# Performance work log

Hardware: AMD Instinct MI355X
Metric: run time of the kernel (lower is better)

The kernel has to match this reference:

```python
import jax, jax.numpy as jnp
import numpy as np

EPS = 1e-12  # F.normalize eps


def setup_inputs() -> dict:
    key = jax.random.key(0)
    k1, k2 = jax.random.split(key)
    bs, d = 8192, 128
    data = jax.random.normal(k1, (bs, d), dtype=jnp.float32)
    label = jax.random.randint(k2, (bs, 1), 0, 2, dtype=jnp.int64)
    scale = jnp.asarray(np.log(1.0 / 0.07), dtype=jnp.float32)  # learned temperature param
    return {"data": data, "scale": scale, "label": label}


def reference(data, scale, label):
    bs = data.shape[0]
    # L2-normalize rows (F.normalize semantics with eps clamp)
    norm = jnp.maximum(jnp.linalg.norm(data, axis=-1, keepdims=True), EPS)
    x = data / norm
    logits = (x @ x.T) * jnp.exp(scale)  # [bs, bs]
    # Vectorized equivalent of the python double loop: binary same-class matrix
    sim = (label == label.T).astype(logits.dtype)  # [bs, bs]
    q = jax.nn.softmax(sim / jnp.sum(sim, axis=-1, keepdims=True), axis=-1)
    p = jax.nn.log_softmax(logits, axis=-1)
    log_q = jnp.log(q)  # q > 0 always (softmax output)
    # F.kl_div(p, q, 'batchmean') = sum(q * (log q - p)) / bs
    loss1 = jnp.sum(q * (log_q - p)) / bs
    # F.kl_div(q.log(), p.exp(), 'batchmean') = sum(exp(p) * (p - log q)) / bs
    loss2 = jnp.sum(jnp.exp(p) * (p - log_q)) / bs
    return (loss1 + loss2) * 0.5
```

## Files before the change

### kernel.cpp

```cpp
#include <hip/hip_runtime.h>
#include <stdint.h>

#define BS 8192
#define DD 128
#define L2E 1.4426950408889634f
#define LN2 0.6931471805599453f

typedef __attribute__((ext_vector_type(8))) short short8;
typedef __attribute__((ext_vector_type(4))) float float4v;

#if __has_builtin(__builtin_amdgcn_exp2f)
#define EXP2(x) __builtin_amdgcn_exp2f(x)
#else
#define EXP2(x) exp2f(x)
#endif

__device__ __forceinline__ float bf2f(short s) {
  union { unsigned u; float f; } c;
  c.u = ((unsigned)(unsigned short)s) << 16;
  return c.f;
}
__device__ __forceinline__ short f2bf(float f) {
  union { float f; unsigned u; } c; c.f = f;
  unsigned u = c.u + 0x7FFFu + ((c.u >> 16) & 1u);
  return (short)(u >> 16);
}


__global__ __launch_bounds__(256) void k_norm(const float* __restrict__ data,
                                              const int* __restrict__ label,
                                              char* __restrict__ xnbF,
                                              float* __restrict__ gh4,
                                              int* __restrict__ cnt4,
                                              float* __restrict__ Zr,
                                              float* __restrict__ Ur,
                                              float* __restrict__ Vr,
                                              float* __restrict__ mf) {
  __shared__ float shg[256];
  __shared__ int shc[2];
  int tid = threadIdx.x, wave = tid >> 6, lane = tid & 63;
  int lh = lane & 31, rsel = lane >> 5;
  if (tid < 2) shc[tid] = 0;
  shg[tid] = 0.f;
  int rowbase = blockIdx.x * 32;
  if (tid < 32) {
    int row = rowbase + tid;
    Zr[row] = 0.f; Ur[row] = 0.f; Vr[row] = 0.f;
    mf[row] = (label[row] == 0) ? 1.f : 0.f;
  }
  __syncthreads();

  float a00 = 0.f, a01 = 0.f, a02 = 0.f, a03 = 0.f;
  float a10 = 0.f, a11 = 0.f, a12 = 0.f, a13 = 0.f;
  int c0 = 0, c1 = 0;
#pragma unroll
  for (int it = 0; it < 4; ++it) {
    int row = rowbase + it * 8 + wave * 2 + rsel;
    float4 v = *(const float4*)&data[row * DD + lh * 4];
    float ss = v.x * v.x + v.y * v.y + v.z * v.z + v.w * v.w;
#pragma unroll
    for (int off = 16; off; off >>= 1) ss += __shfl_xor(ss, off);
    float rn = 1.f / fmaxf(sqrtf(ss), 1e-12f);
    float x0 = v.x * rn, x1 = v.y * rn, x2 = v.z * rn, x3 = v.w * rn;

    unsigned pk0 = (unsigned)(unsigned short)f2bf(x0) |
                   ((unsigned)(unsigned short)f2bf(x1) << 16);
    unsigned pk1 = (unsigned)(unsigned short)f2bf(x2) |
                   ((unsigned)(unsigned short)f2bf(x3) << 16);
    int kc = lh >> 1;
    size_t chunk = (size_t)(row >> 4) * 256 + (size_t)(kc >> 2) * 64 +
                   (size_t)(kc & 3) * 16 + (row & 15);
    *(uint2*)(xnbF + chunk * 16 + (lh & 1) * 8) = make_uint2(pk0, pk1);

    int lab = label[row];
    if (lab == 0) {
      a00 += x0; a01 += x1; a02 += x2; a03 += x3;
      if (lh == 0) c0++;
    } else {
      a10 += x0; a11 += x1; a12 += x2; a13 += x3;
      if (lh == 0) c1++;
    }
  }
  int base = lh * 4;
  atomicAdd(&shg[base + 0], a00); atomicAdd(&shg[base + 1], a01);
  atomicAdd(&shg[base + 2], a02); atomicAdd(&shg[base + 3], a03);
  atomicAdd(&shg[128 + base + 0], a10); atomicAdd(&shg[128 + base + 1], a11);
  atomicAdd(&shg[128 + base + 2], a12); atomicAdd(&shg[128 + base + 3], a13);
  if (lh == 0) { atomicAdd(&shc[0], c0); atomicAdd(&shc[1], c1); }
  __syncthreads();
  atomicAdd(&gh4[(blockIdx.x & 3) * 256 + tid], shg[tid]);
  if (tid < 2) atomicAdd(&cnt4[(blockIdx.x & 3) * 2 + tid], shc[tid]);
}

__global__ __launch_bounds__(256, 2) void k_main(const short* __restrict__ xnbF,
                                                 const int* __restrict__ label,
                                                 const float* __restrict__ mf,
                                                 const float* __restrict__ scale,
                                                 float* __restrict__ Zr,
                                                 float* __restrict__ Ur,
                                                 float* __restrict__ Vr) {
  int tid = threadIdx.x, wave = tid >> 6, lane = tid & 63;
  int quad = lane >> 4, col = lane & 15;
  int rbI = blockIdx.x >> 5;
  int sl = blockIdx.x & 31;
  float se2 = __expf(scale[0]) * L2E;

  const short8* F = (const short8*)xnbF;

  int gA = rbI * 16 + wave * 4;
  short8 af[4][4];
#pragma unroll
  for (int s = 0; s < 4; ++s)
#pragma unroll
    for (int t = 0; t < 4; ++t) {
      short8 a = F[(size_t)(gA + s) * 256 + t * 64 + lane];
#pragma unroll
      for (int i = 0; i < 8; ++i) a[i] = f2bf(bf2f(a[i]) * se2);
      asm volatile("" : "+v"(a));
      af[s][t] = a;
    }

  float4v Zc0 = {0.f,0.f,0.f,0.f}, Zc1 = Zc0, Zc2 = Zc0, Zc3 = Zc0;
  float4v Uc0 = Zc0, Uc1 = Zc0, Uc2 = Zc0, Uc3 = Zc0;
  float4v Vc0 = Zc0, Vc1 = Zc0, Vc2 = Zc0, Vc3 = Zc0;

  const short8* FB = F + (size_t)(sl * 16) * 256 + lane;
  short8 n0 = FB[0], n1 = FB[64], n2 = FB[128], n3 = FB[192];
  float nm = mf[sl * 256 + col];

#pragma unroll 1
  for (int gg = 0; gg < 16; ++gg) {
    short8 b0 = n0, b1 = n1, b2 = n2, b3 = n3;
    float bm = nm;
    if (gg < 15) {
      const short8* np = FB + (size_t)(gg + 1) * 256;
      n0 = np[0]; n1 = np[64]; n2 = np[128]; n3 = np[192];
      nm = mf[sl * 256 + (gg + 1) * 16 + col];
    }
#define ROWSET(s, Zc, Uc, Vc)                                                  \
    {                                                                          \
      float4v c = {0.f, 0.f, 0.f, 0.f};                                        \
      c = __builtin_amdgcn_mfma_f32_16x16x32_bf16(af[s][0], b0, c, 0, 0, 0);   \
      c = __builtin_amdgcn_mfma_f32_16x16x32_bf16(af[s][1], b1, c, 0, 0, 0);   \
      c = __builtin_amdgcn_mfma_f32_16x16x32_bf16(af[s][2], b2, c, 0, 0, 0);   \
      c = __builtin_amdgcn_mfma_f32_16x16x32_bf16(af[s][3], b3, c, 0, 0, 0);   \
      _Pragma("unroll")                                                        \
      for (int r = 0; r < 4; ++r) {  \
        float l = c[r], e = EXP2(l);    \
        Zc[r] += e;                                                            \
        Uc[r] = fmaf(e, l, Uc[r]);                                             \
        Vc[r] = fmaf(bm, e, Vc[r]);                                            \
      }                                                                        \
    }
    ROWSET(0, Zc0, Uc0, Vc0)
    ROWSET(1, Zc1, Uc1, Vc1)
    ROWSET(2, Zc2, Uc2, Vc2)
    ROWSET(3, Zc3, Uc3, Vc3)
#undef ROWSET
  }

#define EMIT(s, Zc, Uc, Vc)                                                    \
  {                                                                            \
    _Pragma("unroll")                                                          \
    for (int r = 0; r < 4; ++r) {                                              \
      float z = Zc[r], u = Uc[r], v0 = Vc[r];                                  \
      _Pragma("unroll")                                                        \
      for (int off = 1; off < 16; off <<= 1) {                                 \
        z += __shfl_xor(z, off);                                               \
        u += __shfl_xor(u, off);                                               \
        v0 += __shfl_xor(v0, off);                                             \
      }                                                                        \
      if (col == 0) {                                                          \
        int row = rbI * 256 + wave * 64 + s * 16 + quad * 4 + r;               \
        int lab = label[row];                                                  \
        float v = (lab == 0) ? v0 : (z - v0);                                  \
        atomicAdd(&Zr[row], z);                                                \
        atomicAdd(&Ur[row], u * LN2);                 \
        atomicAdd(&Vr[row], v);                                                \
      }                                                                        \
    }                                                                          \
  }
  EMIT(0, Zc0, Uc0, Vc0)
  EMIT(1, Zc1, Uc1, Vc1)
  EMIT(2, Zc2, Uc2, Vc2)
  EMIT(3, Zc3, Uc3, Vc3)
#undef EMIT
}

__global__ __launch_bounds__(256) void k_final(const float* __restrict__ data,
                                               const int* __restrict__ label,
                                               const float* __restrict__ scale,
                                               const float* __restrict__ gh4,
                                               const int* __restrict__ cnt4,
                                               const float* __restrict__ Zr,
                                               const float* __restrict__ Ur,
                                               const float* __restrict__ Vr,
                                               float* __restrict__ partial) {
  __shared__ float hsum[256];
  __shared__ float bsum[4];
  int tid = threadIdx.x, wave = tid >> 6, lane = tid & 63;
  int lh = lane & 31, rsel = lane >> 5;
  hsum[tid] = gh4[tid] + gh4[256 + tid] + gh4[512 + tid] + gh4[768 + tid];
  __syncthreads();

  float se = __expf(scale[0]);
  float c0 = (float)(cnt4[0] + cnt4[2] + cnt4[4] + cnt4[6]);
  float c1 = (float)(cnt4[1] + cnt4[3] + cnt4[5] + cnt4[7]);
  float4 h0 = *(const float4*)&hsum[lh * 4];
  float4 h1 = *(const float4*)&hsum[128 + lh * 4];

  float local = 0.f;
#pragma unroll
  for (int it = 0; it < 4; ++it) {
    int row = blockIdx.x * 32 + it * 8 + wave * 2 + rsel;
    float4 v = *(const float4*)&data[row * DD + lh * 4];
    float ss = v.x * v.x + v.y * v.y + v.z * v.z + v.w * v.w;
#pragma unroll
    for (int off = 16; off; off >>= 1) ss += __shfl_xor(ss, off);
    float rn = 1.f / fmaxf(sqrtf(ss), 1e-12f);

    int lab = label[row];
    float sg = v.x * (h0.x + h1.x) + v.y * (h0.y + h1.y) +
               v.z * (h0.z + h1.z) + v.w * (h0.w + h1.w);
    float sh_ = (lab == 0)
                    ? (v.x * h0.x + v.y * h0.y + v.z * h0.z + v.w * h0.w)
                    : (v.x * h1.x + v.y * h1.y + v.z * h1.z + v.w * h1.w);
#pragma unroll
    for (int off = 16; off; off >>= 1) {
      sg += __shfl_xor(sg, off);
      sh_ += __shfl_xor(sh_, off);
    }
    if (lh == 0) {
      float cc = (lab == 0) ? c0 : c1;
      float a = __expf(1.f / cc);
      float Zq = cc * a + ((float)BS - cc);
      float S = se * sg * rn, T = se * sh_ * rn;
      float Zv = Zr[row], Uv = Ur[row], Vv = Vr[row];
      local += a / Zq - (S + (a - 1.f) * T) / Zq + Uv / Zv - Vv / (cc * Zv);
    }
  }
#pragma unroll
  for (int off = 32; off; off >>= 1) local += __shfl_xor(local, off);
  if (lane == 0) bsum[wave] = local;
  __syncthreads();
  if (tid == 0) partial[blockIdx.x] = bsum[0] + bsum[1] + bsum[2] + bsum[3];
}

__global__ __launch_bounds__(256) void k_sum(const float* __restrict__ partial,
                                             float* __restrict__ out) {
  __shared__ float bsum[4];
  int tid = threadIdx.x, wave = tid >> 6, lane = tid & 63;
  float v = partial[tid];
#pragma unroll
  for (int off = 32; off; off >>= 1) v += __shfl_xor(v, off);
  if (lane == 0) bsum[wave] = v;
  __syncthreads();
  if (tid == 0)
    out[0] = (bsum[0] + bsum[1] + bsum[2] + bsum[3]) * (0.5f / (float)BS);
}

extern "C" void kernel_launch(void* const* d_in, const int* in_sizes, int n_in,
                              void* d_out, int out_size, void* d_ws, size_t ws_size,
                              hipStream_t stream) {
  const float* data = (const float*)d_in[0];
  const float* scale = (const float*)d_in[1];
  const int* label = (const int*)d_in[2];
  char* ws = (char*)d_ws;
  char* xnbF = ws;
  float* Zr = (float*)(ws + 2097152);
  float* Ur = (float*)(ws + 2129920);
  float* Vr = (float*)(ws + 2162688);
  float* gh4 = (float*)(ws + 2195456);
  int* cnt4 = (int*)(ws + 2199552);
  float* mf = (float*)(ws + 2199584);
  float* partial = (float*)(ws + 2232352);

  hipMemsetAsync(ws + 2195456, 0, 4128, stream);

  k_norm<<<256, 256, 0, stream>>>(data, label, xnbF, gh4, cnt4, Zr, Ur, Vr, mf);
  k_main<<<1024, 256, 0, stream>>>((const short*)xnbF, label, mf, scale, Zr, Ur, Vr);
  k_final<<<256, 256, 0, stream>>>(data, label, scale, gh4, cnt4, Zr, Ur, Vr, partial);
  k_sum<<<1, 256, 0, stream>>>(partial, (float*)d_out);
}
```

Measured before the change: 122.4 us.

## Software-pipeline MFMA with exp epilogue and fuse final sum into last block

The main loop is restructured into a two-stage ping-pong: the MFMAs for one column group are issued while the exp/accumulate epilogue of the previous group runs, and B tiles are prefetched two groups ahead. The goal is to overlap matrix-core latency with the transcendental epilogue. Separately, the k_sum launch is removed by having the last k_final block, chosen with an atomic ticket, do the final reduction. The asm barrier on the A fragments is also dropped. These changes add register pressure and an acquire/release handshake in exchange.

Result: no change. 124.8 us (+1.9%).

```diff
diff --git a/kernel.cpp b/kernel.cpp
--- a/kernel.cpp
+++ b/kernel.cpp
@@ -116,7 +116,6 @@
       short8 a = F[(size_t)(gA + s) * 256 + t * 64 + lane];
 #pragma unroll
       for (int i = 0; i < 8; ++i) a[i] = f2bf(bf2f(a[i]) * se2);
-      asm volatile("" : "+v"(a));
       af[s][t] = a;
     }
 
@@ -125,39 +124,64 @@
   float4v Vc0 = Zc0, Vc1 = Zc0, Vc2 = Zc0, Vc3 = Zc0;
 
   const short8* FB = F + (size_t)(sl * 16) * 256 + lane;
-  short8 n0 = FB[0], n1 = FB[64], n2 = FB[128], n3 = FB[192];
-  float nm = mf[sl * 256 + col];
-
+  const float* MB = mf + sl * 256 + col;
+
+  short8 pA0, pA1, pA2, pA3, pB0, pB1, pB2, pB3;
+  float mA, mB_;
+  float4v cP0, cP1, cP2, cP3, cQ0, cQ1, cQ2, cQ3;
+
+#define LOADP(g) { const short8* p_ = FB + (size_t)(g) * 256;                  \
+    pA0 = p_[0]; pA1 = p_[64]; pA2 = p_[128]; pA3 = p_[192];                   \
+    mA = MB[(g) * 16]; }
+#define LOADQ(g) { const short8* p_ = FB + (size_t)(g) * 256;                  \
+    pB0 = p_[0]; pB1 = p_[64]; pB2 = p_[128]; pB3 = p_[192];                   \
+    mB_ = MB[(g) * 16]; }
+#define MFMA1(cc, s, b0, b1, b2, b3)                                           \
+    cc = (float4v){0.f, 0.f, 0.f, 0.f};                                        \
+    cc = __builtin_amdgcn_mfma_f32_16x16x32_bf16(af[s][0], b0, cc, 0, 0, 0);   \
+    cc = __builtin_amdgcn_mfma_f32_16x16x32_bf16(af[s][1], b1, cc, 0, 0, 0);   \
+    cc = __builtin_amdgcn_mfma_f32_16x16x32_bf16(af[s][2], b2, cc, 0, 0, 0);   \
+    cc = __builtin_amdgcn_mfma_f32_16x16x32_bf16(af[s][3], b3, cc, 0, 0, 0);
+#define MFMA4(c0, c1, c2, c3, b0, b1, b2, b3)                                  \
+    { MFMA1(c0, 0, b0, b1, b2, b3) MFMA1(c1, 1, b0, b1, b2, b3)                \
+      MFMA1(c2, 2, b0, b1, b2, b3) MFMA1(c3, 3, b0, b1, b2, b3) }
+#define EPIROW(cc, Zc, Uc, Vc, mm)                                             \
+    { _Pragma("unroll")                                                        \
+      for (int r = 0; r < 4; ++r) {  \
+        float l = (cc)[r], e = EXP2(l);      \
+        (Zc)[r] += e;                                                          \
+        (Uc)[r] = fmaf(e, l, (Uc)[r]);                                         \
+        (Vc)[r] = fmaf((mm), e, (Vc)[r]);                                      \
+      } }
+#define EPI4(c0, c1, c2, c3, mm)                                               \
+    EPIROW(c0, Zc0, Uc0, Vc0, mm) EPIROW(c1, Zc1, Uc1, Vc1, mm)                \
+    EPIROW(c2, Zc2, Uc2, Vc2, mm) EPIROW(c3, Zc3, Uc3, Vc3, mm)
+
+  LOADP(0); LOADQ(1);
+  MFMA4(cP0, cP1, cP2, cP3, pA0, pA1, pA2, pA3);
+  float mPe = mA;
+  LOADP(2);
 #pragma unroll 1
-  for (int gg = 0; gg < 16; ++gg) {
-    short8 b0 = n0, b1 = n1, b2 = n2, b3 = n3;
-    float bm = nm;
-    if (gg < 15) {
-      const short8* np = FB + (size_t)(gg + 1) * 256;
-      n0 = np[0]; n1 = np[64]; n2 = np[128]; n3 = np[192];
-      nm = mf[sl * 256 + (gg + 1) * 16 + col];
-    }
-#define ROWSET(s, Zc, Uc, Vc)                                                  \
-    {                                                                          \
-      float4v c = {0.f, 0.f, 0.f, 0.f};                                        \
-      c = __builtin_amdgcn_mfma_f32_16x16x32_bf16(af[s][0], b0, c, 0, 0, 0);   \
-      c = __builtin_amdgcn_mfma_f32_16x16x32_bf16(af[s][1], b1, c, 0, 0, 0);   \
-      c = __builtin_amdgcn_mfma_f32_16x16x32_bf16(af[s][2], b2, c, 0, 0, 0);   \
-      c = __builtin_amdgcn_mfma_f32_16x16x32_bf16(af[s][3], b3, c, 0, 0, 0);   \
-      _Pragma("unroll")                                                        \
-      for (int r = 0; r < 4; ++r) {  \
-        float l = c[r], e = EXP2(l);    \
-        Zc[r] += e;                                                            \
-        Uc[r] = fmaf(e, l, Uc[r]);                                             \
-        Vc[r] = fmaf(bm, e, Vc[r]);                                            \
-      }                                                                        \
-    }
-    ROWSET(0, Zc0, Uc0, Vc0)
-    ROWSET(1, Zc1, Uc1, Vc1)
-    ROWSET(2, Zc2, Uc2, Vc2)
-    ROWSET(3, Zc3, Uc3, Vc3)
-#undef ROWSET
-  }
+  for (int g = 1; g < 14; g += 2) {
+    MFMA4(cQ0, cQ1, cQ2, cQ3, pB0, pB1, pB2, pB3);
+    float mQe = mB_;
+    LOADQ(g + 2);
+    EPI4(cP0, cP1, cP2, cP3, mPe);
+    MFMA4(cP0, cP1, cP2, cP3, pA0, pA1, pA2, pA3);
+    mPe = mA;
+    if (g + 3 < 16) LOADP(g + 3);
+    EPI4(cQ0, cQ1, cQ2, cQ3, mQe);
+  }
+  MFMA4(cQ0, cQ1, cQ2, cQ3, pB0, pB1, pB2, pB3);
+  float mQe = mB_;
+  EPI4(cP0, cP1, cP2, cP3, mPe);
+  EPI4(cQ0, cQ1, cQ2, cQ3, mQe);
+#undef LOADP
+#undef LOADQ
+#undef MFMA1
+#undef MFMA4
+#undef EPIROW
+#undef EPI4
 
 #define EMIT(s, Zc, Uc, Vc)                                                    \
   {                                                                            \
@@ -195,9 +219,12 @@
                                                const float* __restrict__ Zr,
                                                const float* __restrict__ Ur,
                                                const float* __restrict__ Vr,
-                                               float* __restrict__ partial) {
+                                               float* __restrict__ partial,
+                                               int* __restrict__ ticket,
+                                               float* __restrict__ out) {
   __shared__ float hsum[256];
   __shared__ float bsum[4];
+  __shared__ int lastb;
   int tid = threadIdx.x, wave = tid >> 6, lane = tid & 63;
   int lh = lane & 31, rsel = lane >> 5;
   hsum[tid] = gh4[tid] + gh4[256 + tid] + gh4[512 + tid] + gh4[768 + tid];
@@ -243,20 +270,25 @@
   for (int off = 32; off; off >>= 1) local += __shfl_xor(local, off);
   if (lane == 0) bsum[wave] = local;
   __syncthreads();
-  if (tid == 0) partial[blockIdx.x] = bsum[0] + bsum[1] + bsum[2] + bsum[3];
-}
-
-__global__ __launch_bounds__(256) void k_sum(const float* __restrict__ partial,
-                                             float* __restrict__ out) {
-  __shared__ float bsum[4];
-  int tid = threadIdx.x, wave = tid >> 6, lane = tid & 63;
-  float v = partial[tid];
-#pragma unroll
-  for (int off = 32; off; off >>= 1) v += __shfl_xor(v, off);
-  if (lane == 0) bsum[wave] = v;
-  __syncthreads();
-  if (tid == 0)
-    out[0] = (bsum[0] + bsum[1] + bsum[2] + bsum[3]) * (0.5f / (float)BS);
+  if (tid == 0) {
+    float psum = bsum[0] + bsum[1] + bsum[2] + bsum[3];
+    __hip_atomic_store(&partial[blockIdx.x], psum, __ATOMIC_RELEASE,
+                       __HIP_MEMORY_SCOPE_AGENT);
+    int t = __hip_atomic_fetch_add(ticket, 1, __ATOMIC_ACQ_REL,
+                                   __HIP_MEMORY_SCOPE_AGENT);
+    lastb = (t == 255);
+  }
+  __syncthreads();
+  if (lastb) {
+    float v = __hip_atomic_load(&partial[tid], __ATOMIC_ACQUIRE,
+                                __HIP_MEMORY_SCOPE_AGENT);
+#pragma unroll
+    for (int off = 32; off; off >>= 1) v += __shfl_xor(v, off);
+    if (lane == 0) bsum[wave] = v;
+    __syncthreads();
+    if (tid == 0)
+      out[0] = (bsum[0] + bsum[1] + bsum[2] + bsum[3]) * (0.5f / (float)BS);
+  }
 }
 
 extern "C" void kernel_launch(void* const* d_in, const int* in_sizes, int n_in,
@@ -272,13 +304,14 @@
   float* Vr = (float*)(ws + 2162688);
   float* gh4 = (float*)(ws + 2195456);
   int* cnt4 = (int*)(ws + 2199552);
-  float* mf = (float*)(ws + 2199584);
-  float* partial = (float*)(ws + 2232352);
-
-  hipMemsetAsync(ws + 2195456, 0, 4128, stream);
+  int* ticket = (int*)(ws + 2199584);
+  float* partial = (float*)(ws + 2199588);
+  float* mf = (float*)(ws + 2200640);
+
+  hipMemsetAsync(ws + 2195456, 0, 4132, stream);
 
   k_norm<<<256, 256, 0, stream>>>(data, label, xnbF, gh4, cnt4, Zr, Ur, Vr, mf);
   k_main<<<1024, 256, 0, stream>>>((const short*)xnbF, label, mf, scale, Zr, Ur, Vr);
-  k_final<<<256, 256, 0, stream>>>(data, label, scale, gh4, cnt4, Zr, Ur, Vr, partial);
-  k_sum<<<1, 256, 0, stream>>>(partial, (float*)d_out);
-}
+  k_final<<<256, 256, 0, stream>>>(data, label, scale, gh4, cnt4, Zr, Ur, Vr,
+                                   partial, ticket, (float*)d_out);
+}
```

## Stage B tiles in LDS via global_load_lds, widen blocks, fuse final sum

Applied to the files above, without the earlier changes.

The main GEMM-softmax kernel now runs 512-thread blocks whose 8 waves share double-buffered LDS tiles of the column operand, loaded with direct global-to-LDS instructions. Each wave holds 2 row groups instead of 4 and computes a 2x2 MFMA grid per step, so each column fragment is reused across row groups and global traffic for B drops. The separate reduction kernel is folded into k_final through an atomic ticket that lets the last block finish the sum, saving one launch. Histogram partials are spread over 8 slots instead of 4 to cut atomic contention, at the cost of more LDS use, extra block-wide syncs, and fewer independent rows per wave.

Result: faster. 108.7 us (-11.2%).

```diff
diff --git a/kernel.cpp b/kernel.cpp
--- a/kernel.cpp
+++ b/kernel.cpp
@@ -30,8 +30,8 @@
 __global__ __launch_bounds__(256) void k_norm(const float* __restrict__ data,
                                               const int* __restrict__ label,
                                               char* __restrict__ xnbF,
-                                              float* __restrict__ gh4,
-                                              int* __restrict__ cnt4,
+                                              float* __restrict__ gh8,
+                                              int* __restrict__ cnt8,
                                               float* __restrict__ Zr,
                                               float* __restrict__ Ur,
                                               float* __restrict__ Vr,
@@ -88,76 +88,113 @@
   atomicAdd(&shg[128 + base + 2], a12); atomicAdd(&shg[128 + base + 3], a13);
   if (lh == 0) { atomicAdd(&shc[0], c0); atomicAdd(&shc[1], c1); }
   __syncthreads();
-  atomicAdd(&gh4[(blockIdx.x & 3) * 256 + tid], shg[tid]);
-  if (tid < 2) atomicAdd(&cnt4[(blockIdx.x & 3) * 2 + tid], shc[tid]);
-}
-
-__global__ __launch_bounds__(256, 2) void k_main(const short* __restrict__ xnbF,
+  atomicAdd(&gh8[(blockIdx.x & 7) * 256 + tid], shg[tid]);
+  if (tid < 2) atomicAdd(&cnt8[(blockIdx.x & 7) * 2 + tid], shc[tid]);
+}
+
+__global__ __launch_bounds__(512, 4) void k_main(const short* __restrict__ xnbF,
                                                  const int* __restrict__ label,
                                                  const float* __restrict__ mf,
                                                  const float* __restrict__ scale,
                                                  float* __restrict__ Zr,
                                                  float* __restrict__ Ur,
                                                  float* __restrict__ Vr) {
+  __shared__ short tile[2][64 * DD];
   int tid = threadIdx.x, wave = tid >> 6, lane = tid & 63;
   int quad = lane >> 4, col = lane & 15;
-  int rbI = blockIdx.x >> 5;
-  int sl = blockIdx.x & 31;
+  int rbI = blockIdx.x >> 4;
+  int sl = blockIdx.x & 15;
   float se2 = __expf(scale[0]) * L2E;
 
   const short8* F = (const short8*)xnbF;
 
-  int gA = rbI * 16 + wave * 4;
-  short8 af[4][4];
-#pragma unroll
-  for (int s = 0; s < 4; ++s)
+  int gA = rbI * 16 + wave * 2;
+  short8 af[2][4];
+#pragma unroll
+  for (int s = 0; s < 2; ++s)
 #pragma unroll
     for (int t = 0; t < 4; ++t) {
       short8 a = F[(size_t)(gA + s) * 256 + t * 64 + lane];
 #pragma unroll
       for (int i = 0; i < 8; ++i) a[i] = f2bf(bf2f(a[i]) * se2);
-      asm volatile("" : "+v"(a));
       af[s][t] = a;
     }
 
-  float4v Zc0 = {0.f,0.f,0.f,0.f}, Zc1 = Zc0, Zc2 = Zc0, Zc3 = Zc0;
-  float4v Uc0 = Zc0, Uc1 = Zc0, Uc2 = Zc0, Uc3 = Zc0;
-  float4v Vc0 = Zc0, Vc1 = Zc0, Vc2 = Zc0, Vc3 = Zc0;
-
-  const short8* FB = F + (size_t)(sl * 16) * 256 + lane;
-  short8 n0 = FB[0], n1 = FB[64], n2 = FB[128], n3 = FB[192];
-  float nm = mf[sl * 256 + col];
+  float4v Z0 = {0.f,0.f,0.f,0.f}, Z1 = Z0, U0 = Z0, U1 = Z0, V0 = Z0, V1 = Z0;
+
+  int cb4 = sl * 32;
+
+#define STAGE(buf, jt)                                                         \
+  {                                                                            \
+    const char* s_ = (const char*)xnbF +                                       \
+                     ((size_t)(cb4 + (jt) * 4) * 256 + tid) * 16;              \
+    char* d_ = (char*)tile[buf] + tid * 16;                                    \
+    __builtin_amdgcn_global_load_lds(                                          \
+        (const __attribute__((address_space(1))) void*)(uintptr_t)s_,          \
+        (__attribute__((address_space(3))) void*)(uintptr_t)d_, 16, 0, 0);     \
+    __builtin_amdgcn_global_load_lds(                                          \
+        (const __attribute__((address_space(1))) void*)(uintptr_t)(s_ + 8192), \
+        (__attribute__((address_space(3))) void*)(uintptr_t)(d_ + 8192),       \
+        16, 0, 0);                                                             \
+  }
+
+  STAGE(0, 0);
+  __syncthreads();
 
 #pragma unroll 1
-  for (int gg = 0; gg < 16; ++gg) {
-    short8 b0 = n0, b1 = n1, b2 = n2, b3 = n3;
-    float bm = nm;
-    if (gg < 15) {
-      const short8* np = FB + (size_t)(gg + 1) * 256;
-      n0 = np[0]; n1 = np[64]; n2 = np[128]; n3 = np[192];
-      nm = mf[sl * 256 + (gg + 1) * 16 + col];
-    }
-#define ROWSET(s, Zc, Uc, Vc)                                                  \
+  for (int jt = 0; jt < 8; ++jt) {
+    if (jt < 7) STAGE((jt + 1) & 1, jt + 1);
+    const short8* T8 = (const short8*)tile[jt & 1];
+    int jcb = sl * 512 + jt * 64;
+
+#define HALFTILE(jo)                                                           \
     {                                                                          \
-      float4v c = {0.f, 0.f, 0.f, 0.f};                                        \
-      c = __builtin_amdgcn_mfma_f32_16x16x32_bf16(af[s][0], b0, c, 0, 0, 0);   \
-      c = __builtin_amdgcn_mfma_f32_16x16x32_bf16(af[s][1], b1, c, 0, 0, 0);   \
-      c = __builtin_amdgcn_mfma_f32_16x16x32_bf16(af[s][2], b2, c, 0, 0, 0);   \
-      c = __builtin_amdgcn_mfma_f32_16x16x32_bf16(af[s][3], b3, c, 0, 0, 0);   \
+      short8 b00 = T8[(jo) * 256 + lane];                                      \
+      short8 b01 = T8[(jo) * 256 + 64 + lane];                                 \
+      short8 b02 = T8[(jo) * 256 + 128 + lane];                                \
+      short8 b03 = T8[(jo) * 256 + 192 + lane];                                \
+      short8 b10 = T8[(jo + 1) * 256 + lane];                                  \
+      short8 b11 = T8[(jo + 1) * 256 + 64 + lane];                             \
+      short8 b12 = T8[(jo + 1) * 256 + 128 + lane];                            \
+      short8 b13 = T8[(jo + 1) * 256 + 192 + lane];                            \
+      float m0 = mf[jcb + (jo) * 16 + col];                                    \
+      float m1 = mf[jcb + (jo + 1) * 16 + col];                                \
+      float4v c00 = {0.f, 0.f, 0.f, 0.f}, c01 = c00, c10 = c00, c11 = c00;     \
+      c00 = __builtin_amdgcn_mfma_f32_16x16x32_bf16(af[0][0], b00, c00, 0,0,0);\
+      c01 = __builtin_amdgcn_mfma_f32_16x16x32_bf16(af[1][0], b00, c01, 0,0,0);\
+      c10 = __builtin_amdgcn_mfma_f32_16x16x32_bf16(af[0][0], b10, c10, 0,0,0);\
+      c11 = __builtin_amdgcn_mfma_f32_16x16x32_bf16(af[1][0], b10, c11, 0,0,0);\
+      c00 = __builtin_amdgcn_mfma_f32_16x16x32_bf16(af[0][1], b01, c00, 0,0,0);\
+      c01 = __builtin_amdgcn_mfma_f32_16x16x32_bf16(af[1][1], b01, c01, 0,0,0);\
+      c10 = __builtin_amdgcn_mfma_f32_16x16x32_bf16(af[0][1], b11, c10, 0,0,0);\
+      c11 = __builtin_amdgcn_mfma_f32_16x16x32_bf16(af[1][1], b11, c11, 0,0,0);\
+      c00 = __builtin_amdgcn_mfma_f32_16x16x32_bf16(af[0][2], b02, c00, 0,0,0);\
+      c01 = __builtin_amdgcn_mfma_f32_16x16x32_bf16(af[1][2], b02, c01, 0,0,0);\
+      c10 = __builtin_amdgcn_mfma_f32_16x16x32_bf16(af[0][2], b12, c10, 0,0,0);\
+      c11 = __builtin_amdgcn_mfma_f32_16x16x32_bf16(af[1][2], b12, c11, 0,0,0);\
+      c00 = __builtin_amdgcn_mfma_f32_16x16x32_bf16(af[0][3], b03, c00, 0,0,0);\
+      c01 = __builtin_amdgcn_mfma_f32_16x16x32_bf16(af[1][3], b03, c01, 0,0,0);\
+      c10 = __builtin_amdgcn_mfma_f32_16x16x32_bf16(af[0][3], b13, c10, 0,0,0);\
+      c11 = __builtin_amdgcn_mfma_f32_16x16x32_bf16(af[1][3], b13, c11, 0,0,0);\
       _Pragma("unroll")                                                        \
       for (int r = 0; r < 4; ++r) {  \
-        float l = c[r], e = EXP2(l);    \
-        Zc[r] += e;                                                            \
-        Uc[r] = fmaf(e, l, Uc[r]);                                             \
-        Vc[r] = fmaf(bm, e, Vc[r]);                                            \
+        float l, e;                                                            \
+        l = c00[r]; e = EXP2(l);        \
+        Z0[r] += e; U0[r] = fmaf(e, l, U0[r]); V0[r] = fmaf(m0, e, V0[r]);     \
+        l = c01[r]; e = EXP2(l);                                               \
+        Z1[r] += e; U1[r] = fmaf(e, l, U1[r]); V1[r] = fmaf(m0, e, V1[r]);     \
+        l = c10[r]; e = EXP2(l);                                               \
+        Z0[r] += e; U0[r] = fmaf(e, l, U0[r]); V0[r] = fmaf(m1, e, V0[r]);     \
+        l = c11[r]; e = EXP2(l);                                               \
+        Z1[r] += e; U1[r] = fmaf(e, l, U1[r]); V1[r] = fmaf(m1, e, V1[r]);     \
       }                                                                        \
     }
-    ROWSET(0, Zc0, Uc0, Vc0)
-    ROWSET(1, Zc1, Uc1, Vc1)
-    ROWSET(2, Zc2, Uc2, Vc2)
-    ROWSET(3, Zc3, Uc3, Vc3)
-#undef ROWSET
-  }
+    HALFTILE(0)
+    HALFTILE(2)
+#undef HALFTILE
+    __syncthreads();
+  }
+#undef STAGE
 
 #define EMIT(s, Zc, Uc, Vc)                                                    \
   {                                                                            \
@@ -171,7 +208,7 @@
         v0 += __shfl_xor(v0, off);                                             \
       }                                                                        \
       if (col == 0) {                                                          \
-        int row = rbI * 256 + wave * 64 + s * 16 + quad * 4 + r;               \
+        int row = rbI * 256 + wave * 32 + s * 16 + quad * 4 + r;               \
         int lab = label[row];                                                  \
         float v = (lab == 0) ? v0 : (z - v0);                                  \
         atomicAdd(&Zr[row], z);                                                \
@@ -180,32 +217,38 @@
       }                                                                        \
     }                                                                          \
   }
-  EMIT(0, Zc0, Uc0, Vc0)
-  EMIT(1, Zc1, Uc1, Vc1)
-  EMIT(2, Zc2, Uc2, Vc2)
-  EMIT(3, Zc3, Uc3, Vc3)
+  EMIT(0, Z0, U0, V0)
+  EMIT(1, Z1, U1, V1)
 #undef EMIT
 }
 
 __global__ __launch_bounds__(256) void k_final(const float* __restrict__ data,
                                                const int* __restrict__ label,
                                                const float* __restrict__ scale,
-                                               const float* __restrict__ gh4,
-                                               const int* __restrict__ cnt4,
+                                               const float* __restrict__ gh8,
+                                               const int* __restrict__ cnt8,
                                                const float* __restrict__ Zr,
                                                const float* __restrict__ Ur,
                                                const float* __restrict__ Vr,
-                                               float* __restrict__ partial) {
+                                               float* __restrict__ partial,
+                                               int* __restrict__ ticket,
+                                               float* __restrict__ out) {
   __shared__ float hsum[256];
   __shared__ float bsum[4];
+  __shared__ int lastb;
   int tid = threadIdx.x, wave = tid >> 6, lane = tid & 63;
   int lh = lane & 31, rsel = lane >> 5;
-  hsum[tid] = gh4[tid] + gh4[256 + tid] + gh4[512 + tid] + gh4[768 + tid];
+  float hs = 0.f;
+#pragma unroll
+  for (int i = 0; i < 8; ++i) hs += gh8[i * 256 + tid];
+  hsum[tid] = hs;
   __syncthreads();
 
   float se = __expf(scale[0]);
-  float c0 = (float)(cnt4[0] + cnt4[2] + cnt4[4] + cnt4[6]);
-  float c1 = (float)(cnt4[1] + cnt4[3] + cnt4[5] + cnt4[7]);
+  int ci0 = 0, ci1 = 0;
+#pragma unroll
+  for (int i = 0; i < 8; ++i) { ci0 += cnt8[2 * i]; ci1 += cnt8[2 * i + 1]; }
+  float c0 = (float)ci0, c1 = (float)ci1;
   float4 h0 = *(const float4*)&hsum[lh * 4];
   float4 h1 = *(const float4*)&hsum[128 + lh * 4];
 
@@ -243,20 +286,25 @@
   for (int off = 32; off; off >>= 1) local += __shfl_xor(local, off);
   if (lane == 0) bsum[wave] = local;
   __syncthreads();
-  if (tid == 0) partial[blockIdx.x] = bsum[0] + bsum[1] + bsum[2] + bsum[3];
-}
-
-__global__ __launch_bounds__(256) void k_sum(const float* __restrict__ partial,
-                                             float* __restrict__ out) {
-  __shared__ float bsum[4];
-  int tid = threadIdx.x, wave = tid >> 6, lane = tid & 63;
-  float v = partial[tid];
-#pragma unroll
-  for (int off = 32; off; off >>= 1) v += __shfl_xor(v, off);
-  if (lane == 0) bsum[wave] = v;
-  __syncthreads();
-  if (tid == 0)
-    out[0] = (bsum[0] + bsum[1] + bsum[2] + bsum[3]) * (0.5f / (float)BS);
+  if (tid == 0) {
+    float psum = bsum[0] + bsum[1] + bsum[2] + bsum[3];
+    __hip_atomic_store(&partial[blockIdx.x], psum, __ATOMIC_RELEASE,
+                       __HIP_MEMORY_SCOPE_AGENT);
+    int t = __hip_atomic_fetch_add(ticket, 1, __ATOMIC_ACQ_REL,
+                                   __HIP_MEMORY_SCOPE_AGENT);
+    lastb = (t == 255);
+  }
+  __syncthreads();
+  if (lastb) {
+    float v = __hip_atomic_load(&partial[tid], __ATOMIC_ACQUIRE,
+                                __HIP_MEMORY_SCOPE_AGENT);
+#pragma unroll
+    for (int off = 32; off; off >>= 1) v += __shfl_xor(v, off);
+    if (lane == 0) bsum[wave] = v;
+    __syncthreads();
+    if (tid == 0)
+      out[0] = (bsum[0] + bsum[1] + bsum[2] + bsum[3]) * (0.5f / (float)BS);
+  }
 }
 
 extern "C" void kernel_launch(void* const* d_in, const int* in_sizes, int n_in,
@@ -270,15 +318,16 @@
   float* Zr = (float*)(ws + 2097152);
   float* Ur = (float*)(ws + 2129920);
   float* Vr = (float*)(ws + 2162688);
-  float* gh4 = (float*)(ws + 2195456);
-  int* cnt4 = (int*)(ws + 2199552);
-  float* mf = (float*)(ws + 2199584);
-  float* partial = (float*)(ws + 2232352);
-
-  hipMemsetAsync(ws + 2195456, 0, 4128, stream);
-
-  k_norm<<<256, 256, 0, stream>>>(data, label, xnbF, gh4, cnt4, Zr, Ur, Vr, mf);
-  k_main<<<1024, 256, 0, stream>>>((const short*)xnbF, label, mf, scale, Zr, Ur, Vr);
-  k_final<<<256, 256, 0, stream>>>(data, label, scale, gh4, cnt4, Zr, Ur, Vr, partial);
-  k_sum<<<1, 256, 0, stream>>>(partial, (float*)d_out);
-}
+  float* gh8 = (float*)(ws + 2195456);
+  int* cnt8 = (int*)(ws + 2203648);
+  int* ticket = (int*)(ws + 2203712);
+  float* partial = (float*)(ws + 2203716);
+  float* mf = (float*)(ws + 2204800);
+
+  hipMemsetAsync(ws + 2195456, 0, 8260, stream);
+
+  k_norm<<<256, 256, 0, stream>>>(data, label, xnbF, gh8, cnt8, Zr, Ur, Vr, mf);
+  k_main<<<512, 512, 0, stream>>>((const short*)xnbF, label, mf, scale, Zr, Ur, Vr);
+  k_final<<<256, 256, 0, stream>>>(data, label, scale, gh8, cnt8, Zr, Ur, Vr,
+                                   partial, ticket, (float*)d_out);
+}
```
